# Kernel tuning notes

Hardware: AMD Instinct MI355X
Metric: run time of the kernel (lower is better)

## Reference

```python
import jax, jax.numpy as jnp
import numpy as np

B, N, D, H, C = 2048, 6, 2048, 1024, 200  # batch, nodes/graph, feat dim, hidden, classes
ALPHA = 0.015   # distance decay in edge weight
SCALE = 24.0    # weight rescale after mean-subtraction + clamp


def setup_inputs() -> dict:
    key = jax.random.key(0)
    k1, k2, k3, k4 = jax.random.split(key, 4)
    part_feats = jax.random.normal(k1, (B, N, D), dtype=jnp.float32)
    # cdds columns: [score, y0, x0, y1, x1, idx]; only cols 1:5 (box coords) are used
    cdds = jax.random.uniform(k2, (B, N, 6), dtype=jnp.float32) * 448.0
    fc_w = jax.random.normal(k3, (2 * D, H), dtype=jnp.float32) * 0.02
    fc_b = jnp.zeros((H,), dtype=jnp.float32)
    cls_w = jax.random.normal(k4, (H, C), dtype=jnp.float32) * 0.02
    cls_b = jnp.zeros((C,), dtype=jnp.float32)
    return {"part_feats": part_feats, "cdds": cdds, "fc_w": fc_w, "fc_b": fc_b,
            "cls_w": cls_w, "cls_b": cls_b}


def reference(part_feats, cdds, fc_w, fc_b, cls_w, cls_b):
    # --- edge weights on per-sample complete graph (apply_edges) ---
    loc = cdds[:, :, 1:5]                      # (B, N, 4) = (y0, x0, y1, x1)
    cy = (loc[..., 0] + loc[..., 2]) * 0.5     # node center y, (B, N)
    cx = (loc[..., 1] + loc[..., 3]) * 0.5     # node center x, (B, N)
    dx = cx[:, :, None] - cx[:, None, :]       # (B, N, N) pairwise
    dy = cy[:, :, None] - cy[:, None, :]
    d2 = dx * dx + dy * dy
    mask = ~jnp.eye(N, dtype=bool)             # off-diagonal = real edges (30 per graph)
    dist = jnp.sqrt(jnp.where(mask, d2, 1.0))  # safe sqrt off the diagonal
    w0 = jnp.where(mask, jnp.exp(-ALPHA * dist), 0.0)
    mean_w = jnp.sum(w0, axis=(1, 2), keepdims=True) / (N * (N - 1))  # mean over 30 edges
    w = SCALE * jnp.maximum(w0 - mean_w, 0.0) * mask                  # (B, N, N), w[b,u,v]
    # --- update_all: u_mul_e + mean over the (N-1) incoming edges per node ---
    hidden = jnp.einsum('buv,bud->bvd', w, part_feats) / (N - 1)      # (B, N, D)
    # --- node MLP + graph mean readout + classifier ---
    node_ft = jnp.concatenate([hidden, part_feats], axis=-1) @ fc_w + fc_b  # (B, N, H)
    g_ft = node_ft.mean(axis=1)                                             # (B, H)
    return g_ft @ cls_w + cls_b                                             # (B, C)
```

## Files before the change

### kernel.cpp

```cpp
#include <hip/hip_runtime.h>
#include <math.h>

namespace {
constexpr int NB = 2048;
constexpr int NNODE = 6;
constexpr int DD = 2048;
constexpr int HH = 1024;
constexpr int CC = 200;
constexpr int K2 = 2 * DD;
constexpr int NPAD = 256;
constexpr int ZS1 = 4;
constexpr int ZS2 = 16;
constexpr float ALPHA_C = 0.015f;
constexpr float SCALE_C = 24.0f;
}

typedef __attribute__((ext_vector_type(8))) short bf16x8;
typedef __attribute__((ext_vector_type(4))) float f32x4;

static __device__ __forceinline__ unsigned short f2bf(float x) {
    union { float f; unsigned int u; } v; v.f = x;
    unsigned int r = v.u + 0x7FFFu + ((v.u >> 16) & 1u);
    return (unsigned short)(r >> 16);
}

static __device__ __forceinline__ float bf2f(unsigned short u) {
    union { unsigned int i; float f; } v; v.i = ((unsigned int)u) << 16;
    return v.f;
}

static __device__ __forceinline__ void compute_s_wave(const float* __restrict__ cdds,
                                                      int b, float sv[NNODE]) {
    const int lane = threadIdx.x & 63;
    const int u = lane >> 3;
    const int v = lane & 7;
    const float* cd = cdds + (size_t)b * 36;
    float w = 0.f;
    const bool valid = (u < 6) & (v < 6) & (u != v);
    if (u < 6 && v < 6 && u != v) {
        float cyu = (cd[u * 6 + 1] + cd[u * 6 + 3]) * 0.5f;
        float cxu = (cd[u * 6 + 2] + cd[u * 6 + 4]) * 0.5f;
        float cyv = (cd[v * 6 + 1] + cd[v * 6 + 3]) * 0.5f;
        float cxv = (cd[v * 6 + 2] + cd[v * 6 + 4]) * 0.5f;
        float dx = cxu - cxv, dy = cyu - cyv;
        w = expf(-ALPHA_C * sqrtf(dx * dx + dy * dy));
    }
    float s = w;
#pragma unroll
    for (int m = 32; m >= 1; m >>= 1) s += __shfl_xor(s, m);
    float mean = s * (1.f / 30.f);
    float tt = valid ? fmaxf(w - mean, 0.f) : 0.f;
    tt += __shfl_xor(tt, 1);
    tt += __shfl_xor(tt, 2);
    tt += __shfl_xor(tt, 4);
    float su = SCALE_C * tt * 0.2f;
#pragma unroll
    for (int uu = 0; uu < NNODE; ++uu) sv[uu] = __shfl(su, uu * 8);
}

__global__ __launch_bounds__(256) void k_cvt(const float* __restrict__ cls_w,
                                             unsigned short* __restrict__ cls_wT)
{
    __shared__ float sm[64 * 65];
    const int kt = blockIdx.x & 15;
    const int nt = blockIdx.x >> 4;
    const int t = threadIdx.x;
#pragma unroll
    for (int c = 0; c < 4; ++c) {
        int i = t + c * 256;
        int kr = i >> 4;
        int n4 = (i & 15) << 2;
        int gn = nt * 64 + n4;
        const float* sp = cls_w + (size_t)(kt * 64 + kr) * CC + gn;
        float4 v = {0.f, 0.f, 0.f, 0.f};
        if (gn + 3 < CC) {
            v = *(const float4*)sp;
        } else {
            if (gn + 0 < CC) v.x = sp[0];
            if (gn + 1 < CC) v.y = sp[1];
            if (gn + 2 < CC) v.z = sp[2];
            if (gn + 3 < CC) v.w = sp[3];
        }
        sm[kr * 65 + n4 + 0] = v.x; sm[kr * 65 + n4 + 1] = v.y;
        sm[kr * 65 + n4 + 2] = v.z; sm[kr * 65 + n4 + 3] = v.w;
    }
    __syncthreads();
#pragma unroll
    for (int c = 0; c < 4; ++c) {
        int i = t + c * 256;
        int nr = i >> 4;
        int k4 = (i & 15) << 2;
        ushort4 o;
        o.x = f2bf(sm[(k4 + 0) * 65 + nr]);
        o.y = f2bf(sm[(k4 + 1) * 65 + nr]);
        o.z = f2bf(sm[(k4 + 2) * 65 + nr]);
        o.w = f2bf(sm[(k4 + 3) * 65 + nr]);
        *(ushort4*)(cls_wT + (size_t)(nt * 64 + nr) * HH + kt * 64 + k4) = o;
    }
}

__global__ __launch_bounds__(256) void k_g1(const float* __restrict__ fc_w,
                                            const unsigned short* __restrict__ Bt,
                                            float* __restrict__ partM)
{
    __shared__ short As[32][72];
    __shared__ short Bs[256][72];
    const int t = threadIdx.x;
    const int lane = t & 63;
    const int wid = t >> 6;
    const int bm = blockIdx.x * 32;
    const int z = blockIdx.y;
    const int kbase = z * (HH / ZS1);

    f32x4 acc[2][4] = {};

    for (int k0 = kbase; k0 < kbase + HH / ZS1; k0 += 64) {
#pragma unroll
        for (int c = 0; c < 2; ++c) {
            int i = t + c * 256;
            int row = i >> 4;
            int k4 = (i & 15) << 2;
            float4 v = *(const float4*)(fc_w + (size_t)(bm + row) * HH + k0 + k4);
            ushort4 o;
            o.x = f2bf(v.x); o.y = f2bf(v.y); o.z = f2bf(v.z); o.w = f2bf(v.w);
            *(ushort4*)&As[row][k4] = o;
        }
#pragma unroll
        for (int c = 0; c < 8; ++c) {
            int i = t + c * 256;
            int n = i >> 3;
            int k8 = (i & 7) << 3;
            *(uint4*)&Bs[n][k8] =
                *(const uint4*)(Bt + (size_t)n * HH + k0 + k8);
        }
        __syncthreads();
#pragma unroll
        for (int ks = 0; ks < 2; ++ks) {
            int kk = ks * 32 + ((lane >> 4) << 3);
            int ar = lane & 15;
            bf16x8 a0 = *(const bf16x8*)&As[ar][kk];
            bf16x8 a1 = *(const bf16x8*)&As[16 + ar][kk];
#pragma unroll
            for (int fn = 0; fn < 4; ++fn) {
                bf16x8 b = *(const bf16x8*)&Bs[wid * 64 + fn * 16 + ar][kk];
                acc[0][fn] = __builtin_amdgcn_mfma_f32_16x16x32_bf16(a0, b, acc[0][fn], 0, 0, 0);
                acc[1][fn] = __builtin_amdgcn_mfma_f32_16x16x32_bf16(a1, b, acc[1][fn], 0, 0, 0);
            }
        }
        __syncthreads();
    }
#pragma unroll
    for (int fm = 0; fm < 2; ++fm)
#pragma unroll
        for (int fn = 0; fn < 4; ++fn) {
            int gm0 = bm + fm * 16 + ((lane >> 4) << 2);
            int gn = wid * 64 + fn * 16 + (lane & 15);
#pragma unroll
            for (int r = 0; r < 4; ++r)
                partM[((size_t)z * K2 + gm0 + r) * NPAD + gn] = acc[fm][fn][r];
        }
}

__global__ __launch_bounds__(256) void k_red(const float* __restrict__ partM,
                                             const float* __restrict__ cls_w,
                                             const float* __restrict__ fc_b,
                                             const float* __restrict__ cls_b,
                                             unsigned short* __restrict__ Mt,
                                             float* __restrict__ bvec)
{
    __shared__ float sm[64][69];
    __shared__ float red[256];
    const int bx = blockIdx.x;
    const int t = threadIdx.x;

    if (bx >= 256) {
        const int bb = bx - 256;
        int c8 = t & 7;
        int hs = t >> 3;
        int c = bb * 8 + c8;
        float acc = 0.f;
        for (int h = hs; h < HH; h += 32)
            acc += fc_b[h] * cls_w[(size_t)h * CC + c];
        red[t] = acc;
        __syncthreads();
        for (int s = 128; s >= 8; s >>= 1) {
            if (t < s) red[t] += red[t + s];
            __syncthreads();
        }
        if (t < 8) bvec[c] = red[t] + cls_b[c];
        return;
    }

    const int bm = (bx >> 2) * 64;
    const int bn = (bx & 3) * 64;
#pragma unroll
    for (int c = 0; c < 4; ++c) {
        int i = t + c * 256;
        int mr = i >> 4;
        int n4 = (i & 15) << 2;
        float4 s = {0.f, 0.f, 0.f, 0.f};
#pragma unroll
        for (int z = 0; z < ZS1; ++z) {
            float4 v = *(const float4*)(partM +
                ((size_t)z * K2 + bm + mr) * NPAD + bn + n4);
            s.x += v.x; s.y += v.y; s.z += v.z; s.w += v.w;
        }
        sm[mr][n4 + 0] = s.x; sm[mr][n4 + 1] = s.y;
        sm[mr][n4 + 2] = s.z; sm[mr][n4 + 3] = s.w;
    }
    __syncthreads();
#pragma unroll
    for (int c = 0; c < 4; ++c) {
        int i = t + c * 256;
        int nr = i >> 4;
        int m4 = (i & 15) << 2;
        ushort4 o;
        o.x = f2bf(sm[m4 + 0][nr]);
        o.y = f2bf(sm[m4 + 1][nr]);
        o.z = f2bf(sm[m4 + 2][nr]);
        o.w = f2bf(sm[m4 + 3][nr]);
        *(ushort4*)(Mt + (size_t)(bn + nr) * K2 + bm + m4) = o;
    }
}

__global__ __launch_bounds__(256) void k_pq(const float* __restrict__ pf,
                                            const float* __restrict__ cdds,
                                            unsigned short* __restrict__ pq)
{
    const int bid = blockIdx.x;
    const int b = bid >> 1;
    const int d = ((bid & 1) << 10) + (threadIdx.x << 2);

    const float* base = pf + (size_t)b * NNODE * DD + d;
    float4 v0 = *(const float4*)(base + 0 * DD);
    float4 v1 = *(const float4*)(base + 1 * DD);
    float4 v2 = *(const float4*)(base + 2 * DD);
    float4 v3 = *(const float4*)(base + 3 * DD);
    float4 v4 = *(const float4*)(base + 4 * DD);
    float4 v5 = *(const float4*)(base + 5 * DD);

    float sv[NNODE];
    compute_s_wave(cdds, b, sv);

    float4 q;
    q.x = v0.x + v1.x + v2.x + v3.x + v4.x + v5.x;
    q.y = v0.y + v1.y + v2.y + v3.y + v4.y + v5.y;
    q.z = v0.z + v1.z + v2.z + v3.z + v4.z + v5.z;
    q.w = v0.w + v1.w + v2.w + v3.w + v4.w + v5.w;

    float4 p = {0.f, 0.f, 0.f, 0.f};
    p.x = fmaf(sv[0], v0.x, p.x); p.y = fmaf(sv[0], v0.y, p.y);
    p.z = fmaf(sv[0], v0.z, p.z); p.w = fmaf(sv[0], v0.w, p.w);
    p.x = fmaf(sv[1], v1.x, p.x); p.y = fmaf(sv[1], v1.y, p.y);
    p.z = fmaf(sv[1], v1.z, p.z); p.w = fmaf(sv[1], v1.w, p.w);
    p.x = fmaf(sv[2], v2.x, p.x); p.y = fmaf(sv[2], v2.y, p.y);
    p.z = fmaf(sv[2], v2.z, p.z); p.w = fmaf(sv[2], v2.w, p.w);
    p.x = fmaf(sv[3], v3.x, p.x); p.y = fmaf(sv[3], v3.y, p.y);
    p.z = fmaf(sv[3], v3.z, p.z); p.w = fmaf(sv[3], v3.w, p.w);
    p.x = fmaf(sv[4], v4.x, p.x); p.y = fmaf(sv[4], v4.y, p.y);
    p.z = fmaf(sv[4], v4.z, p.z); p.w = fmaf(sv[4], v4.w, p.w);
    p.x = fmaf(sv[5], v5.x, p.x); p.y = fmaf(sv[5], v5.y, p.y);
    p.z = fmaf(sv[5], v5.z, p.z); p.w = fmaf(sv[5], v5.w, p.w);

    unsigned short* o = pq + (size_t)b * K2;
    ushort4 pb, qb;
    pb.x = f2bf(p.x); pb.y = f2bf(p.y); pb.z = f2bf(p.z); pb.w = f2bf(p.w);
    qb.x = f2bf(q.x); qb.y = f2bf(q.y); qb.z = f2bf(q.z); qb.w = f2bf(q.w);
    *(ushort4*)(o + d) = pb;
    *(ushort4*)(o + DD + d) = qb;
}

__global__ __launch_bounds__(256) void k_gemm2(const unsigned short* __restrict__ A,
                                               const unsigned short* __restrict__ Bt,
                                               unsigned short* __restrict__ part)
{
    __shared__ short As[64][72];
    __shared__ short Bs[256][72];
    const int t = threadIdx.x;
    const int lane = t & 63;
    const int wid = t >> 6;
    const int wr = wid >> 1, wc = wid & 1;
    const int bm = blockIdx.x * 64;
    const int z = blockIdx.y;
    const int kbase = z * (K2 / ZS2);

    f32x4 acc[2][8] = {};

    for (int k0 = kbase; k0 < kbase + K2 / ZS2; k0 += 64) {
#pragma unroll
        for (int c = 0; c < 2; ++c) {
            int i = t + c * 256;
            int row = i >> 3;
            int k8 = (i & 7) << 3;
            *(uint4*)&As[row][k8] =
                *(const uint4*)(A + (size_t)(bm + row) * K2 + k0 + k8);
        }
#pragma unroll
        for (int c = 0; c < 8; ++c) {
            int i = t + c * 256;
            int n = i >> 3;
            int k8 = (i & 7) << 3;
            *(uint4*)&Bs[n][k8] =
                *(const uint4*)(Bt + (size_t)n * K2 + k0 + k8);
        }
        __syncthreads();
#pragma unroll
        for (int ks = 0; ks < 2; ++ks) {
            int kk = ks * 32 + ((lane >> 4) << 3);
            int ar = lane & 15;
            bf16x8 a0 = *(const bf16x8*)&As[wr * 32 + ar][kk];
            bf16x8 a1 = *(const bf16x8*)&As[wr * 32 + 16 + ar][kk];
#pragma unroll
            for (int fn = 0; fn < 8; ++fn) {
                bf16x8 b = *(const bf16x8*)&Bs[wc * 128 + fn * 16 + ar][kk];
                acc[0][fn] = __builtin_amdgcn_mfma_f32_16x16x32_bf16(a0, b, acc[0][fn], 0, 0, 0);
                acc[1][fn] = __builtin_amdgcn_mfma_f32_16x16x32_bf16(a1, b, acc[1][fn], 0, 0, 0);
            }
        }
        __syncthreads();
    }
#pragma unroll
    for (int fm = 0; fm < 2; ++fm)
#pragma unroll
        for (int fn = 0; fn < 8; ++fn) {
            int gm0 = bm + wr * 32 + fm * 16 + ((lane >> 4) << 2);
            int gn = wc * 128 + fn * 16 + (lane & 15);
#pragma unroll
            for (int r = 0; r < 4; ++r)
                part[((size_t)z * NB + gm0 + r) * NPAD + gn] = f2bf(acc[fm][fn][r]);
        }
}

__global__ __launch_bounds__(256) void k_combine(const unsigned short* __restrict__ part,
                                                 const float* __restrict__ bvec,
                                                 float* __restrict__ out)
{
    int idx = blockIdx.x * blockDim.x + threadIdx.x;
    if (idx >= NB * (CC / 4)) return;
    int b = idx / (CC / 4);
    int c0 = (idx - b * (CC / 4)) << 2;
    float s0 = 0.f, s1 = 0.f, s2 = 0.f, s3 = 0.f;
#pragma unroll
    for (int z = 0; z < ZS2; ++z) {
        ushort4 v = *(const ushort4*)(part + ((size_t)z * NB + b) * NPAD + c0);
        s0 += bf2f(v.x); s1 += bf2f(v.y); s2 += bf2f(v.z); s3 += bf2f(v.w);
    }
    float4 o;
    o.x = s0 * (1.f / 6.f) + bvec[c0 + 0];
    o.y = s1 * (1.f / 6.f) + bvec[c0 + 1];
    o.z = s2 * (1.f / 6.f) + bvec[c0 + 2];
    o.w = s3 * (1.f / 6.f) + bvec[c0 + 3];
    *(float4*)(out + (size_t)b * CC + c0) = o;
}

extern "C" void kernel_launch(void* const* d_in, const int* in_sizes, int n_in,
                              void* d_out, int out_size, void* d_ws, size_t ws_size,
                              hipStream_t stream)
{
    const float* part_feats = (const float*)d_in[0];
    const float* cdds = (const float*)d_in[1];
    const float* fc_w = (const float*)d_in[2];
    const float* fc_b = (const float*)d_in[3];
    const float* cls_w = (const float*)d_in[4];
    const float* cls_b = (const float*)d_in[5];
    float* out = (float*)d_out;

    char* ws = (char*)d_ws;
    size_t off = 0;
    unsigned short* pq = (unsigned short*)(ws + off);     off += (size_t)NB * K2 * 2;
    unsigned short* Mt = (unsigned short*)(ws + off);     off += (size_t)NPAD * K2 * 2;
    unsigned short* cls_wT = (unsigned short*)(ws + off); off += (size_t)NPAD * HH * 2;
    float* partM = (float*)(ws + off);                    off += (size_t)ZS1 * K2 * NPAD * 4;
    unsigned short* part = (unsigned short*)(ws + off);   off += (size_t)ZS2 * NB * NPAD * 2;
    float* bvec = (float*)(ws + off);                     off += 256 * 4;

    k_cvt<<<dim3(64), dim3(256), 0, stream>>>(cls_w, cls_wT);
    k_pq<<<dim3(NB * 2), dim3(256), 0, stream>>>(part_feats, cdds, pq);
    k_g1<<<dim3(K2 / 32, ZS1), dim3(256), 0, stream>>>(fc_w, cls_wT, partM);
    k_red<<<dim3(256 + 25), dim3(256), 0, stream>>>(partM, cls_w, fc_b, cls_b, Mt, bvec);
    k_gemm2<<<dim3(NB / 64, ZS2), dim3(256), 0, stream>>>(pq, Mt, part);
    k_combine<<<dim3((NB * (CC / 4) + 255) / 256), dim3(256), 0, stream>>>(part, bvec, out);
}
```

Measured before the change: 75.91 us.

## Drop split-K in weight-product GEMM and fold bias vector into convert kernel

The fc_w·cls_w product GEMM (k_g1) now runs the full K=1024 loop per block and writes the bf16 transposed result directly, instead of four split-K fp32 partials followed by a separate reduction/transpose kernel. The bias-vector computation moves into the cls_w conversion kernel as extra blocks. This removes one kernel launch and the fp32 partial-buffer round trip through memory, but cuts k_g1's grid from 512 to 128 blocks, each doing four times the serial K work.

```diff
diff --git a/kernel.cpp b/kernel.cpp
--- a/kernel.cpp
+++ b/kernel.cpp
@@ -9,7 +9,6 @@
 constexpr int CC = 200;
 constexpr int K2 = 2 * DD;
 constexpr int NPAD = 256;
-constexpr int ZS1 = 4;
 constexpr int ZS2 = 16;
 constexpr float ALPHA_C = 0.015f;
 constexpr float SCALE_C = 24.0f;
@@ -59,12 +58,34 @@
 }
 
 __global__ __launch_bounds__(256) void k_cvt(const float* __restrict__ cls_w,
-                                             unsigned short* __restrict__ cls_wT)
+                                             const float* __restrict__ fc_b,
+                                             const float* __restrict__ cls_b,
+                                             unsigned short* __restrict__ cls_wT,
+                                             float* __restrict__ bvec)
 {
     __shared__ float sm[64 * 65];
-    const int kt = blockIdx.x & 15;
-    const int nt = blockIdx.x >> 4;
+    const int bx = blockIdx.x;
     const int t = threadIdx.x;
+    if (bx >= 64) {
+        const int bb = bx - 64;
+        float* red = sm;
+        int c8 = t & 7;
+        int hs = t >> 3;
+        int c = bb * 8 + c8;
+        float acc = 0.f;
+        for (int h = hs; h < HH; h += 32)
+            acc += fc_b[h] * cls_w[(size_t)h * CC + c];
+        red[t] = acc;
+        __syncthreads();
+        for (int s = 128; s >= 8; s >>= 1) {
+            if (t < s) red[t] += red[t + s];
+            __syncthreads();
+        }
+        if (t < 8) bvec[c] = red[t] + cls_b[c];
+        return;
+    }
+    const int kt = bx & 15;
+    const int nt = bx >> 4;
 #pragma unroll
     for (int c = 0; c < 4; ++c) {
         int i = t + c * 256;
@@ -99,130 +120,6 @@
     }
 }
 
-__global__ __launch_bounds__(256) void k_g1(const float* __restrict__ fc_w,
-                                            const unsigned short* __restrict__ Bt,
-                                            float* __restrict__ partM)
-{
-    __shared__ short As[32][72];
-    __shared__ short Bs[256][72];
-    const int t = threadIdx.x;
-    const int lane = t & 63;
-    const int wid = t >> 6;
-    const int bm = blockIdx.x * 32;
-    const int z = blockIdx.y;
-    const int kbase = z * (HH / ZS1);
-
-    f32x4 acc[2][4] = {};
-
-    for (int k0 = kbase; k0 < kbase + HH / ZS1; k0 += 64) {
-#pragma unroll
-        for (int c = 0; c < 2; ++c) {
-            int i = t + c * 256;
-            int row = i >> 4;
-            int k4 = (i & 15) << 2;
-            float4 v = *(const float4*)(fc_w + (size_t)(bm + row) * HH + k0 + k4);
-            ushort4 o;
-            o.x = f2bf(v.x); o.y = f2bf(v.y); o.z = f2bf(v.z); o.w = f2bf(v.w);
-            *(ushort4*)&As[row][k4] = o;
-        }
-#pragma unroll
-        for (int c = 0; c < 8; ++c) {
-            int i = t + c * 256;
-            int n = i >> 3;
-            int k8 = (i & 7) << 3;
-            *(uint4*)&Bs[n][k8] =
-                *(const uint4*)(Bt + (size_t)n * HH + k0 + k8);
-        }
-        __syncthreads();
-#pragma unroll
-        for (int ks = 0; ks < 2; ++ks) {
-            int kk = ks * 32 + ((lane >> 4) << 3);
-            int ar = lane & 15;
-            bf16x8 a0 = *(const bf16x8*)&As[ar][kk];
-            bf16x8 a1 = *(const bf16x8*)&As[16 + ar][kk];
-#pragma unroll
-            for (int fn = 0; fn < 4; ++fn) {
-                bf16x8 b = *(const bf16x8*)&Bs[wid * 64 + fn * 16 + ar][kk];
-                acc[0][fn] = __builtin_amdgcn_mfma_f32_16x16x32_bf16(a0, b, acc[0][fn], 0, 0, 0);
-                acc[1][fn] = __builtin_amdgcn_mfma_f32_16x16x32_bf16(a1, b, acc[1][fn], 0, 0, 0);
-            }
-        }
-        __syncthreads();
-    }
-#pragma unroll
-    for (int fm = 0; fm < 2; ++fm)
-#pragma unroll
-        for (int fn = 0; fn < 4; ++fn) {
-            int gm0 = bm + fm * 16 + ((lane >> 4) << 2);
-            int gn = wid * 64 + fn * 16 + (lane & 15);
-#pragma unroll
-            for (int r = 0; r < 4; ++r)
-                partM[((size_t)z * K2 + gm0 + r) * NPAD + gn] = acc[fm][fn][r];
-        }
-}
-
-__global__ __launch_bounds__(256) void k_red(const float* __restrict__ partM,
-                                             const float* __restrict__ cls_w,
-                                             const float* __restrict__ fc_b,
-                                             const float* __restrict__ cls_b,
-                                             unsigned short* __restrict__ Mt,
-                                             float* __restrict__ bvec)
-{
-    __shared__ float sm[64][69];
-    __shared__ float red[256];
-    const int bx = blockIdx.x;
-    const int t = threadIdx.x;
-
-    if (bx >= 256) {
-        const int bb = bx - 256;
-        int c8 = t & 7;
-        int hs = t >> 3;
-        int c = bb * 8 + c8;
-        float acc = 0.f;
-        for (int h = hs; h < HH; h += 32)
-            acc += fc_b[h] * cls_w[(size_t)h * CC + c];
-        red[t] = acc;
-        __syncthreads();
-        for (int s = 128; s >= 8; s >>= 1) {
-            if (t < s) red[t] += red[t + s];
-            __syncthreads();
-        }
-        if (t < 8) bvec[c] = red[t] + cls_b[c];
-        return;
-    }
-
-    const int bm = (bx >> 2) * 64;
-    const int bn = (bx & 3) * 64;
-#pragma unroll
-    for (int c = 0; c < 4; ++c) {
-        int i = t + c * 256;
-        int mr = i >> 4;
-        int n4 = (i & 15) << 2;
-        float4 s = {0.f, 0.f, 0.f, 0.f};
-#pragma unroll
-        for (int z = 0; z < ZS1; ++z) {
-            float4 v = *(const float4*)(partM +
-                ((size_t)z * K2 + bm + mr) * NPAD + bn + n4);
-            s.x += v.x; s.y += v.y; s.z += v.z; s.w += v.w;
-        }
-        sm[mr][n4 + 0] = s.x; sm[mr][n4 + 1] = s.y;
-        sm[mr][n4 + 2] = s.z; sm[mr][n4 + 3] = s.w;
-    }
-    __syncthreads();
-#pragma unroll
-    for (int c = 0; c < 4; ++c) {
-        int i = t + c * 256;
-        int nr = i >> 4;
-        int m4 = (i & 15) << 2;
-        ushort4 o;
-        o.x = f2bf(sm[m4 + 0][nr]);
-        o.y = f2bf(sm[m4 + 1][nr]);
-        o.z = f2bf(sm[m4 + 2][nr]);
-        o.w = f2bf(sm[m4 + 3][nr]);
-        *(ushort4*)(Mt + (size_t)(bn + nr) * K2 + bm + m4) = o;
-    }
-}
-
 __global__ __launch_bounds__(256) void k_pq(const float* __restrict__ pf,
                                             const float* __restrict__ cdds,
                                             unsigned short* __restrict__ pq)
@@ -270,6 +167,67 @@
     *(ushort4*)(o + DD + d) = qb;
 }
 
+__global__ __launch_bounds__(256) void k_g1(const float* __restrict__ fc_w,
+                                            const unsigned short* __restrict__ Bt,
+                                            unsigned short* __restrict__ Mt)
+{
+    __shared__ short As[32][72];
+    __shared__ short Bs[256][72];
+    const int t = threadIdx.x;
+    const int lane = t & 63;
+    const int wid = t >> 6;
+    const int bm = blockIdx.x * 32;
+
+    f32x4 acc[2][4] = {};
+
+    for (int k0 = 0; k0 < HH; k0 += 64) {
+#pragma unroll
+        for (int c = 0; c < 2; ++c) {
+            int i = t + c * 256;
+            int row = i >> 4;
+            int k4 = (i & 15) << 2;
+            float4 v = *(const float4*)(fc_w + (size_t)(bm + row) * HH + k0 + k4);
+            ushort4 o;
+            o.x = f2bf(v.x); o.y = f2bf(v.y); o.z = f2bf(v.z); o.w = f2bf(v.w);
+            *(ushort4*)&As[row][k4] = o;
+        }
+#pragma unroll
+        for (int c = 0; c < 8; ++c) {
+            int i = t + c * 256;
+            int n = i >> 3;
+            int k8 = (i & 7) << 3;
+            *(uint4*)&Bs[n][k8] =
+                *(const uint4*)(Bt + (size_t)n * HH + k0 + k8);
+        }
+        __syncthreads();
+#pragma unroll
+        for (int ks = 0; ks < 2; ++ks) {
+            int kk = ks * 32 + ((lane >> 4) << 3);
+            int ar = lane & 15;
+            bf16x8 a0 = *(const bf16x8*)&As[ar][kk];
+            bf16x8 a1 = *(const bf16x8*)&As[16 + ar][kk];
+#pragma unroll
+            for (int fn = 0; fn < 4; ++fn) {
+                bf16x8 b = *(const bf16x8*)&Bs[wid * 64 + fn * 16 + ar][kk];
+                acc[0][fn] = __builtin_amdgcn_mfma_f32_16x16x32_bf16(a0, b, acc[0][fn], 0, 0, 0);
+                acc[1][fn] = __builtin_amdgcn_mfma_f32_16x16x32_bf16(a1, b, acc[1][fn], 0, 0, 0);
+            }
+        }
+        __syncthreads();
+    }
+#pragma unroll
+    for (int fm = 0; fm < 2; ++fm)
+#pragma unroll
+        for (int fn = 0; fn < 4; ++fn) {
+            int gm0 = bm + fm * 16 + ((lane >> 4) << 2);
+            int gn = wid * 64 + fn * 16 + (lane & 15);
+            ushort4 o;
+            o.x = f2bf(acc[fm][fn][0]); o.y = f2bf(acc[fm][fn][1]);
+            o.z = f2bf(acc[fm][fn][2]); o.w = f2bf(acc[fm][fn][3]);
+            *(ushort4*)(Mt + (size_t)gn * K2 + gm0) = o;
+        }
+}
+
 __global__ __launch_bounds__(256) void k_gemm2(const unsigned short* __restrict__ A,
                                                const unsigned short* __restrict__ Bt,
                                                unsigned short* __restrict__ part)
@@ -370,14 +328,12 @@
     unsigned short* pq = (unsigned short*)(ws + off);     off += (size_t)NB * K2 * 2;
     unsigned short* Mt = (unsigned short*)(ws + off);     off += (size_t)NPAD * K2 * 2;
     unsigned short* cls_wT = (unsigned short*)(ws + off); off += (size_t)NPAD * HH * 2;
-    float* partM = (float*)(ws + off);                    off += (size_t)ZS1 * K2 * NPAD * 4;
     unsigned short* part = (unsigned short*)(ws + off);   off += (size_t)ZS2 * NB * NPAD * 2;
     float* bvec = (float*)(ws + off);                     off += 256 * 4;
 
-    k_cvt<<<dim3(64), dim3(256), 0, stream>>>(cls_w, cls_wT);
+    k_cvt<<<dim3(64 + 25), dim3(256), 0, stream>>>(cls_w, fc_b, cls_b, cls_wT, bvec);
     k_pq<<<dim3(NB * 2), dim3(256), 0, stream>>>(part_feats, cdds, pq);
-    k_g1<<<dim3(K2 / 32, ZS1), dim3(256), 0, stream>>>(fc_w, cls_wT, partM);
-    k_red<<<dim3(256 + 25), dim3(256), 0, stream>>>(partM, cls_w, fc_b, cls_b, Mt, bvec);
+    k_g1<<<dim3(K2 / 32), dim3(256), 0, stream>>>(fc_w, cls_wT, Mt);
     k_gemm2<<<dim3(NB / 64, ZS2), dim3(256), 0, stream>>>(pq, Mt, part);
     k_combine<<<dim3((NB * (CC / 4) + 255) / 256), dim3(256), 0, stream>>>(part, bvec, out);
 }
```

Result: slower. 79.22 us (+4.4%).
